# Kernel tuning notes

Measured on AMD Instinct MI355X. Metric: run time of the kernel, lower is better.

## Reference

```python
import jax, jax.numpy as jnp
import numpy as np

D_MODEL = 1024
N_HEADS = 16
HEAD_DIM = D_MODEL // N_HEADS
WINDOW = 128
NEG = -1e9


def setup_inputs() -> dict:
    key = jax.random.key(0)
    ks = jax.random.split(key, 9)
    s = 1.0 / np.sqrt(D_MODEL)
    x = jax.random.normal(ks[0], (1, 4096, D_MODEL), dtype=jnp.float32)
    Wq = jax.random.uniform(ks[1], (D_MODEL, D_MODEL), jnp.float32, -s, s)
    bq = jax.random.uniform(ks[2], (D_MODEL,), jnp.float32, -s, s)
    Wk = jax.random.uniform(ks[3], (D_MODEL, D_MODEL), jnp.float32, -s, s)
    bk = jax.random.uniform(ks[4], (D_MODEL,), jnp.float32, -s, s)
    Wv = jax.random.uniform(ks[5], (D_MODEL, D_MODEL), jnp.float32, -s, s)
    bv = jax.random.uniform(ks[6], (D_MODEL,), jnp.float32, -s, s)
    Wo = jax.random.uniform(ks[7], (D_MODEL, D_MODEL), jnp.float32, -s, s)
    bo = jax.random.uniform(ks[8], (D_MODEL,), jnp.float32, -s, s)
    return {"x": x, "Wq": Wq, "bq": bq, "Wk": Wk, "bk": bk,
            "Wv": Wv, "bv": bv, "Wo": Wo, "bo": bo}


def reference(x, Wq, bq, Wk, bk, Wv, bv, Wo, bo):
    B, S, _ = x.shape
    scale = 1.0 / np.sqrt(HEAD_DIM)

    def heads(W, b):
        # [B,S,D] -> [B,H,S,hd]  (torch Linear: x @ W.T + b)
        return (x @ W.T + b).reshape(B, S, N_HEADS, HEAD_DIM).transpose(0, 2, 1, 3)

    q = heads(Wq, bq)
    k = heads(Wk, bk)
    v = heads(Wv, bv)

    scores = jnp.einsum('bhqd,bhkd->bhqk', q, k) * scale  # [B,H,S,S]
    i = jnp.arange(S)
    window_mask = jnp.abs(i[:, None] - i[None, :]) <= (WINDOW // 2)  # [S,S]
    scores = jnp.where(window_mask[None, None], scores, NEG)
    attn = jax.nn.softmax(scores, axis=-1)
    ctx = jnp.einsum('bhqk,bhkd->bhqd', attn, v)
    ctx = ctx.transpose(0, 2, 1, 3).reshape(B, S, D_MODEL)
    return ctx @ Wo.T + bo
```

## Files before the change

### kernel.cpp

```cpp
#include <hip/hip_runtime.h>
#include <type_traits>

typedef __bf16 bf16;
typedef __bf16 bf16x8 __attribute__((ext_vector_type(8)));
typedef __bf16 bf16x4 __attribute__((ext_vector_type(4)));
typedef float floatx4 __attribute__((ext_vector_type(4)));

#define SEQ 4096
#define DM 1024
#define NH 16
#define HD 64
#define GUARD 64

__device__ __forceinline__ floatx4 mfma32(bf16x8 a, bf16x8 b, floatx4 c) {
    return __builtin_amdgcn_mfma_f32_16x16x32_bf16(a, b, c, 0, 0, 0);
}

__device__ __forceinline__ bf16x8 load8(const bf16* p) {
    return *(const bf16x8*)p;
}

__device__ __forceinline__ void async_ld16(const bf16* g, bf16* l) {
    __builtin_amdgcn_global_load_lds(
        (const __attribute__((address_space(1))) unsigned int*)g,
        (__attribute__((address_space(3))) unsigned int*)l,
        16, 0, 0);
}

__global__ __launch_bounds__(256) void prep_kernel(
    const float* __restrict__ x,  const float* __restrict__ Wq,
    const float* __restrict__ Wk, const float* __restrict__ Wv,
    const float* __restrict__ Wo, const float* __restrict__ bq,
    const float* __restrict__ bk, const float* __restrict__ bv,
    bf16* __restrict__ xb, bf16* __restrict__ Wcat,
    bf16* __restrict__ Wob, float* __restrict__ bcat)
{
    const int WN8 = 131072;
    const int XN8 = 524288;
    int b = blockIdx.x;
    if (b == 4096) {
        for (int k = threadIdx.x; k < 3 * DM; k += 256)
            bcat[k] = k < DM ? bq[k] : (k < 2 * DM ? bk[k - DM] : bv[k - 2 * DM]);
        return;
    }
    int c = b * 256 + threadIdx.x;
    const float* src; bf16* dst;
    if (c < XN8)              { src = x;  dst = xb; }
    else if (c < XN8 + WN8)   { src = Wq; dst = Wcat;                 c -= XN8; }
    else if (c < XN8 + 2*WN8) { src = Wk; dst = Wcat + (size_t)DM*DM;     c -= XN8 + WN8; }
    else if (c < XN8 + 3*WN8) { src = Wv; dst = Wcat + (size_t)2*DM*DM;   c -= XN8 + 2*WN8; }
    else                      { src = Wo; dst = Wob;                  c -= XN8 + 3*WN8; }
    float4 a = ((const float4*)src)[2 * c], d2 = ((const float4*)src)[2 * c + 1];
    bf16x8 o;
    o[0] = (bf16)a.x;  o[1] = (bf16)a.y;  o[2] = (bf16)a.z;  o[3] = (bf16)a.w;
    o[4] = (bf16)d2.x; o[5] = (bf16)d2.y; o[6] = (bf16)d2.z; o[7] = (bf16)d2.w;
    *(bf16x8*)(dst + 8 * (size_t)c) = o;
}

__global__ __launch_bounds__(256, 3) void gemm_qkv_kernel(
    const bf16* __restrict__ A,
    const bf16* __restrict__ B,
    const float* __restrict__ bias,
    bf16* __restrict__ Qh, bf16* __restrict__ Kh, bf16* __restrict__ Vt)
{
    constexpr int K = DM;
    __shared__ bf16 As[128 * 64];
    __shared__ bf16 Bs[128 * 64];

    const int tid  = threadIdx.x;
    const int wave = tid >> 6;
    const int lane = tid & 63;
    const int l15  = lane & 15;
    const int quad = lane >> 4;
    const int m0 = blockIdx.x * 128;
    const int n0 = blockIdx.y * 128;
    const int wm = (wave & 1) * 64;
    const int wn = (wave >> 1) * 64;

    const int lr = lane >> 3;
    const int gc = ((lane & 7) - lr) & 7;

    const bf16* aptr[4]; bf16* alds[4];
    const bf16* bptr[4]; bf16* blds[4];
#pragma unroll
    for (int i = 0; i < 4; ++i) {
        int ci = wave + 4 * i;
        aptr[i] = A + (size_t)(m0 + ci * 8 + lr) * K + gc * 8;
        alds[i] = As + ci * 512;
        bptr[i] = B + (size_t)(n0 + ci * 8 + lr) * K + gc * 8;
        blds[i] = Bs + ci * 512;
    }

    floatx4 acc[4][4] = {};
    const int sw0 = (quad + (l15 & 7)) & 7;
    const bool qk = (n0 < 2 * DM);

    auto kloop = [&](auto swtag) {
        constexpr bool SW = decltype(swtag)::value;
        for (int k0 = 0; k0 < K; k0 += 64) {
            __syncthreads();
#pragma unroll
            for (int i = 0; i < 4; ++i) async_ld16(aptr[i] + k0, alds[i]);
#pragma unroll
            for (int i = 0; i < 4; ++i) async_ld16(bptr[i] + k0, blds[i]);
            __syncthreads();
#pragma unroll
            for (int h = 0; h < 2; ++h) {
                const int so = ((sw0 + 4 * h) & 7) * 8;
                bf16x8 af[4], bfr[4];
#pragma unroll
                for (int i = 0; i < 4; ++i)
                    af[i] = load8(As + (wm + i * 16 + l15) * 64 + so);
#pragma unroll
                for (int j = 0; j < 4; ++j)
                    bfr[j] = load8(Bs + (wn + j * 16 + l15) * 64 + so);
#pragma unroll
                for (int i = 0; i < 4; ++i)
#pragma unroll
                    for (int j = 0; j < 4; ++j)
                        acc[i][j] = SW ? mfma32(bfr[j], af[i], acc[i][j])
                                       : mfma32(af[i], bfr[j], acc[i][j]);
            }
        }
    };
    if (qk) kloop(std::true_type{}); else kloop(std::false_type{});

    const int nb = n0 + wn;
    if (qk) {
        bf16* dst = (nb < DM) ? Qh : Kh;
        const int hh = ((nb < DM) ? nb : nb - DM) >> 6;
#pragma unroll
        for (int i = 0; i < 4; ++i) {
            int s = m0 + wm + i * 16 + l15;
            bf16* row = dst + ((size_t)hh * SEQ + s) * 64;
#pragma unroll
            for (int j = 0; j < 4; ++j) {
                int d4 = j * 16 + quad * 4;
                float4 bv = *(const float4*)(bias + nb + d4);
                bf16x4 o = {(bf16)(acc[i][j][0] + bv.x), (bf16)(acc[i][j][1] + bv.y),
                            (bf16)(acc[i][j][2] + bv.z), (bf16)(acc[i][j][3] + bv.w)};
                *(bf16x4*)(row + d4) = o;
            }
        }
    } else {
#pragma unroll
        for (int j = 0; j < 4; ++j) {
            int vrow = (nb - 2 * DM) + j * 16 + l15;
            float bvs = bias[nb + j * 16 + l15];
            bf16* row = Vt + (size_t)vrow * SEQ;
#pragma unroll
            for (int i = 0; i < 4; ++i) {
                int s4 = m0 + wm + i * 16 + quad * 4;
                bf16x4 o = {(bf16)(acc[i][j][0] + bvs), (bf16)(acc[i][j][1] + bvs),
                            (bf16)(acc[i][j][2] + bvs), (bf16)(acc[i][j][3] + bvs)};
                *(bf16x4*)(row + s4) = o;
            }
        }
    }
}

template <int BM, typename TOUT>
__global__ __launch_bounds__(256, 4) void gemm_sw_kernel(
    const bf16* __restrict__ A, const bf16* __restrict__ B,
    const float* __restrict__ bias, TOUT* __restrict__ C,
    int M, int N, int K)
{
    constexpr int MI = BM / 32;
    __shared__ bf16 As[BM * 64];
    __shared__ bf16 Bs[128 * 64];

    const int tid  = threadIdx.x;
    const int wave = tid >> 6;
    const int lane = tid & 63;
    const int l15  = lane & 15;
    const int quad = lane >> 4;
    const int m0 = blockIdx.x * BM;
    const int n0 = blockIdx.y * 128;
    const int wm = (wave & 1) * (BM / 2);
    const int wn = (wave >> 1) * 64;

    const int lr = lane >> 3;
    const int gc = ((lane & 7) - lr) & 7;

    const bf16* aptr[MI]; bf16* alds[MI];
    const bf16* bptr[4];  bf16* blds[4];
#pragma unroll
    for (int i = 0; i < MI; ++i) {
        int ci = wave + 4 * i;
        aptr[i] = A + (size_t)(m0 + ci * 8 + lr) * K + gc * 8;
        alds[i] = As + ci * 512;
    }
#pragma unroll
    for (int j = 0; j < 4; ++j) {
        int cj = wave + 4 * j;
        bptr[j] = B + (size_t)(n0 + cj * 8 + lr) * K + gc * 8;
        blds[j] = Bs + cj * 512;
    }

    floatx4 acc[MI][4] = {};
    const int sw0 = (quad + (l15 & 7)) & 7;

    for (int k0 = 0; k0 < K; k0 += 64) {
        __syncthreads();
#pragma unroll
        for (int i = 0; i < MI; ++i) async_ld16(aptr[i] + k0, alds[i]);
#pragma unroll
        for (int j = 0; j < 4; ++j) async_ld16(bptr[j] + k0, blds[j]);
        __syncthreads();
#pragma unroll
        for (int h = 0; h < 2; ++h) {
            const int so = ((sw0 + 4 * h) & 7) * 8;
            bf16x8 af[MI], bfr[4];
#pragma unroll
            for (int i = 0; i < MI; ++i)
                af[i] = load8(As + (wm + i * 16 + l15) * 64 + so);
#pragma unroll
            for (int j = 0; j < 4; ++j)
                bfr[j] = load8(Bs + (wn + j * 16 + l15) * 64 + so);
#pragma unroll
            for (int i = 0; i < MI; ++i)
#pragma unroll
                for (int j = 0; j < 4; ++j)
                    acc[i][j] = mfma32(bfr[j], af[i], acc[i][j]);
        }
    }

#pragma unroll
    for (int i = 0; i < MI; ++i) {
        int xm = m0 + wm + i * 16 + l15;
#pragma unroll
        for (int j = 0; j < 4; ++j) {
            int cn = n0 + wn + j * 16 + quad * 4;
            float4 bv = *(const float4*)(bias + cn);
            float v0 = acc[i][j][0] + bv.x;
            float v1 = acc[i][j][1] + bv.y;
            float v2 = acc[i][j][2] + bv.z;
            float v3 = acc[i][j][3] + bv.w;
            if constexpr (sizeof(TOUT) == 2) {
                bf16x4 o = {(bf16)v0, (bf16)v1, (bf16)v2, (bf16)v3};
                *(bf16x4*)((bf16*)C + (size_t)xm * N + cn) = o;
            } else {
                float4 o = {v0, v1, v2, v3};
                *(float4*)((float*)C + (size_t)xm * N + cn) = o;
            }
        }
    }
}

__global__ __launch_bounds__(256) void swattn_kernel(
    const bf16* __restrict__ Qh, const bf16* __restrict__ Kh,
    const bf16* __restrict__ Vt, bf16* __restrict__ ctx)
{
    __shared__ bf16 Pc[4][16][40];
    __shared__ float lred[4][16];

    const int tid  = threadIdx.x;
    const int wave = tid >> 6;
    const int lane = tid & 63;
    const int l15  = lane & 15;
    const int quad = lane >> 4;
    const int q0   = blockIdx.x * 64;
    const int h    = blockIdx.y;
    const int hoff = h * HD;

    const bf16* qhead = Qh + (size_t)h * SEQ * 64;
    const bf16* khead = Kh + (size_t)h * SEQ * 64;
    const bf16* vhead = Vt + (size_t)hoff * SEQ;

    const int qrow = q0 + wave * 16 + l15;
    bf16x8 aq0 = load8(qhead + (size_t)qrow * 64 + quad * 8);
    bf16x8 aq1 = load8(qhead + (size_t)qrow * 64 + quad * 8 + 32);

    const int ws = q0 - 64 + wave * 16;
    floatx4 s[9];
#pragma unroll
    for (int st = 0; st < 9; ++st) {
        int kr = ws + st * 16 + l15;
        int kc2 = kr < 0 ? 0 : (kr > SEQ - 1 ? SEQ - 1 : kr);
        const bf16* kp = khead + (size_t)kc2 * 64 + quad * 8;
        bf16x8 b0 = load8(kp), b1 = load8(kp + 32);
        floatx4 acc = {};
        acc = mfma32(aq0, b0, acc);
        acc = mfma32(aq1, b1, acc);
        s[st] = acc;
    }

#pragma unroll
    for (int r = 0; r < 4; ++r) {
        int row = quad * 4 + r;
        float mx = -INFINITY;
#pragma unroll
        for (int st = 0; st < 9; ++st) {
            int j = st * 16 + l15;
            int gk = ws + j;
            bool ok = (j >= row) && (j <= 128 + row) && (gk >= 0) && (gk < SEQ);
            float v = ok ? s[st][r] * 0.125f : -1e30f;
            s[st][r] = v;
            mx = fmaxf(mx, v);
        }
        mx = fmaxf(mx, __shfl_xor(mx, 1));
        mx = fmaxf(mx, __shfl_xor(mx, 2));
        mx = fmaxf(mx, __shfl_xor(mx, 4));
        mx = fmaxf(mx, __shfl_xor(mx, 8));
        float sum = 0.f;
#pragma unroll
        for (int st = 0; st < 9; ++st) {
            float p = __expf(s[st][r] - mx);
            s[st][r] = p;
            sum += p;
        }
        sum += __shfl_xor(sum, 1);
        sum += __shfl_xor(sum, 2);
        sum += __shfl_xor(sum, 4);
        sum += __shfl_xor(sum, 8);
        lred[wave][row] = sum;
    }

    floatx4 ot[4] = {};
#pragma unroll
    for (int kc = 0; kc < 5; ++kc) {
#pragma unroll
        for (int r = 0; r < 4; ++r) {
            int row = quad * 4 + r;
            Pc[wave][row][l15] = (bf16)s[2 * kc][r];
            Pc[wave][row][16 + l15] = (kc < 4) ? (bf16)s[2 * kc + 1][r] : (bf16)0.f;
        }
        bf16x8 pb = load8(&Pc[wave][l15][quad * 8]);
#pragma unroll
        for (int dt = 0; dt < 4; ++dt) {
            const bf16* vp = vhead + (ptrdiff_t)(dt * 16 + l15) * SEQ
                                   + (ptrdiff_t)(ws + kc * 32 + quad * 8);
            ot[dt] = mfma32(load8(vp), pb, ot[dt]);
        }
    }

    float linv = 1.0f / lred[wave][l15];
#pragma unroll
    for (int dt = 0; dt < 4; ++dt) {
        bf16x4 o4;
#pragma unroll
        for (int r = 0; r < 4; ++r) o4[r] = (bf16)(ot[dt][r] * linv);
        *(bf16x4*)(ctx + (size_t)qrow * DM + hoff + dt * 16 + quad * 4) = o4;
    }
}

extern "C" void kernel_launch(void* const* d_in, const int* in_sizes, int n_in,
                              void* d_out, int out_size, void* d_ws, size_t ws_size,
                              hipStream_t stream) {
    const float* x  = (const float*)d_in[0];
    const float* Wq = (const float*)d_in[1];
    const float* bq = (const float*)d_in[2];
    const float* Wk = (const float*)d_in[3];
    const float* bk = (const float*)d_in[4];
    const float* Wv = (const float*)d_in[5];
    const float* bv = (const float*)d_in[6];
    const float* Wo = (const float*)d_in[7];
    const float* bo = (const float*)d_in[8];
    float* out = (float*)d_out;

    const size_t XN = (size_t)SEQ * DM;
    const size_t WN = (size_t)DM * DM;

    bf16* xb    = (bf16*)d_ws;
    bf16* Wcat  = xb + XN;
    bf16* Wob   = Wcat + 3 * WN;
    bf16* Qh    = Wob + WN;
    bf16* Kh    = Qh + XN;
    bf16* VtRaw = Kh + XN;
    bf16* Vtb   = VtRaw + GUARD;
    float* bcat = (float*)(VtRaw + XN + 2 * GUARD + 128);
    bf16* ctx   = xb;

    prep_kernel<<<4097, 256, 0, stream>>>(x, Wq, Wk, Wv, Wo, bq, bk, bv,
                                          xb, Wcat, Wob, bcat);

    gemm_qkv_kernel<<<dim3(SEQ / 128, 24), 256, 0, stream>>>(
        xb, Wcat, bcat, Qh, Kh, Vtb);

    swattn_kernel<<<dim3(SEQ / 64, NH), 256, 0, stream>>>(Qh, Kh, Vtb, ctx);

    gemm_sw_kernel<64, float><<<dim3(SEQ / 64, DM / 128), 256, 0, stream>>>(
        ctx, Wob, bo, out, SEQ, DM, DM);
}
```

Baseline: 162.0 us.

## Swizzle block mapping for XCD locality and prefetch V fragments in attention

Remaps block indices in the QKV GEMM and the sliding-window attention kernel so that blocks landing on the same XCD share A/B tiles or neighbouring heads and query ranges, aiming to improve L2 reuse. In attention, V fragments are software-prefetched one chunk ahead, with the first chunk issued before the softmax so global load latency overlaps compute. MFMA sections are wrapped in raised wave priority. The remapping hardcodes grid dimensions (32x24 GEMM tiles, 64x16 attention blocks), and the prefetch buffers add register pressure.

```diff
diff --git a/kernel.cpp b/kernel.cpp
--- a/kernel.cpp
+++ b/kernel.cpp
@@ -72,8 +72,11 @@
     const int lane = tid & 63;
     const int l15  = lane & 15;
     const int quad = lane >> 4;
-    const int m0 = blockIdx.x * 128;
-    const int n0 = blockIdx.y * 128;
+    const int lid = blockIdx.y * 32 + blockIdx.x;
+    const int xcd = lid & 7;
+    const int rr  = lid >> 3;
+    const int m0 = ((xcd & 3) * 8 + (rr & 7)) * 128;
+    const int n0 = ((xcd >> 2) * 12 + (rr >> 3)) * 128;
     const int wm = (wave & 1) * 64;
     const int wn = (wave >> 1) * 64;
 
@@ -259,8 +262,10 @@
     const int lane = tid & 63;
     const int l15  = lane & 15;
     const int quad = lane >> 4;
-    const int q0   = blockIdx.x * 64;
-    const int h    = blockIdx.y;
+    const int lid  = blockIdx.y * 64 + blockIdx.x;
+    const int swz  = (lid & 7) * 128 + (lid >> 3);
+    const int q0   = (swz & 63) * 64;
+    const int h    = swz >> 6;
     const int hoff = h * HD;
 
     const bf16* qhead = Qh + (size_t)h * SEQ * 64;
@@ -285,6 +290,12 @@
         s[st] = acc;
     }
 
+    const bf16* vbase = vhead + (ptrdiff_t)l15 * SEQ + (ws + quad * 8);
+    bf16x8 vf[4];
+#pragma unroll
+    for (int dt = 0; dt < 4; ++dt)
+        vf[dt] = load8(vbase + (ptrdiff_t)dt * 16 * SEQ);
+
 #pragma unroll
     for (int r = 0; r < 4; ++r) {
         int row = quad * 4 + r;
@@ -326,12 +337,18 @@
             Pc[wave][row][16 + l15] = (kc < 4) ? (bf16)s[2 * kc + 1][r] : (bf16)0.f;
         }
         bf16x8 pb = load8(&Pc[wave][l15][quad * 8]);
-#pragma unroll
-        for (int dt = 0; dt < 4; ++dt) {
-            const bf16* vp = vhead + (ptrdiff_t)(dt * 16 + l15) * SEQ
-                                   + (ptrdiff_t)(ws + kc * 32 + quad * 8);
-            ot[dt] = mfma32(load8(vp), pb, ot[dt]);
-        }
+        bf16x8 vcur[4];
+#pragma unroll
+        for (int dt = 0; dt < 4; ++dt) vcur[dt] = vf[dt];
+        if (kc < 4) {
+#pragma unroll
+            for (int dt = 0; dt < 4; ++dt)
+                vf[dt] = load8(vbase + (ptrdiff_t)dt * 16 * SEQ + (kc + 1) * 32);
+        }
+        __builtin_amdgcn_s_setprio(1);
+#pragma unroll
+        for (int dt = 0; dt < 4; ++dt) ot[dt] = mfma32(vcur[dt], pb, ot[dt]);
+        __builtin_amdgcn_s_setprio(0);
     }
 
     float linv = 1.0f / lred[wave][l15];
```

Result: no change. 164.5 us (+1.6%).
